# Kernel optimization log

Hardware: AMD Instinct MI355X
Metric: run time of the kernel (lower is better)

## Reference

```python
import jax, jax.numpy as jnp
import numpy as np

D_MODEL = 768
N_HEADS = 12
HEAD_DIM = D_MODEL // N_HEADS


def setup_inputs() -> dict:
    key = jax.random.key(0)
    k_x, k_wqkv, k_bqkv, k_wo, k_bo = jax.random.split(key, 5)
    s = 1.0 / np.sqrt(D_MODEL)
    return {
        "x": jax.random.normal(k_x, (4, 2048, D_MODEL), dtype=jnp.float32),
        "W_qkv": jax.random.uniform(k_wqkv, (D_MODEL, 3 * D_MODEL), jnp.float32, -s, s),
        "b_qkv": jax.random.uniform(k_bqkv, (3 * D_MODEL,), jnp.float32, -s, s),
        "W_out": jax.random.uniform(k_wo, (D_MODEL, D_MODEL), jnp.float32, -s, s),
        "b_out": jax.random.uniform(k_bo, (D_MODEL,), jnp.float32, -s, s),
    }


def reference(x, W_qkv, b_qkv, W_out, b_out):
    B, S, D = x.shape
    qkv = x @ W_qkv + b_qkv  # [B, S, 3D]
    q, k, v = jnp.split(qkv, 3, axis=-1)

    def heads(t):
        return t.reshape(B, S, N_HEADS, HEAD_DIM).transpose(0, 2, 1, 3)  # [B,H,S,Dh]

    q, k, v = heads(q), heads(k), heads(v)
    scale = HEAD_DIM ** -0.5
    scores = jnp.einsum("bhqd,bhkd->bhqk", q, k) * scale  # [B,H,S,S]
    causal = jnp.tril(jnp.ones((S, S), dtype=bool))
    scores = jnp.where(causal, scores, -jnp.inf)
    probs = jax.nn.softmax(scores, axis=-1)
    out = jnp.einsum("bhqk,bhkd->bhqd", probs, v)  # [B,H,S,Dh]
    out = out.transpose(0, 2, 1, 3).reshape(B, S, D)
    return out @ W_out + b_out
```

## Files before the change

kernel.cpp:

```cpp
#include <hip/hip_runtime.h>
#include <hip/hip_bf16.h>

#define D_MODEL 768
#define NH 12
#define HD 64
#define BATCH 4
#define SEQ 2048
#define BHN (BATCH*NH)
#define MROWS (BATCH*SEQ)

typedef unsigned short u16;
typedef unsigned int u32;
typedef __attribute__((ext_vector_type(8))) short short8;
typedef __attribute__((ext_vector_type(4))) float f32x4;

__device__ inline u16 f2bf(float f){
  union { __hip_bfloat16 h; u16 u; } cv; cv.h = __float2bfloat16(f); return cv.u;
}
__device__ inline u32 pack_bf2(float a, float b){
  return (u32)f2bf(a) | ((u32)f2bf(b) << 16);
}

__device__ inline void async_copy16(const void* g, void* l){
  __builtin_amdgcn_global_load_lds(
      (const __attribute__((address_space(1))) void*)g,
      (__attribute__((address_space(3))) void*)l, 16, 0, 0);
}

__global__ void cast4_kernel(const float* __restrict__ in, u16* __restrict__ out, int n4){
  int i = blockIdx.x*blockDim.x + threadIdx.x;
  if (i < n4){
    const float4 v = ((const float4*)in)[i];
    ushort4 o;
    o.x = f2bf(v.x); o.y = f2bf(v.y); o.z = f2bf(v.z); o.w = f2bf(v.w);
    ((ushort4*)out)[i] = o;
  }
}

__global__ void transpose_cast_kernel(const float* __restrict__ w, u16* __restrict__ wt,
                                      int K, int N){
  __shared__ u16 tile[64][65];
  int k0 = blockIdx.x*64, n0 = blockIdx.y*64;
  int c = threadIdx.x & 63, r0 = threadIdx.x >> 6;
  #pragma unroll
  for (int r = r0; r < 64; r += 4)
    tile[c][r] = f2bf(w[(size_t)(k0+r)*N + n0 + c]);
  __syncthreads();
  #pragma unroll
  for (int r = r0; r < 64; r += 4)
    wt[(size_t)(n0+r)*K + k0 + c] = tile[r][c];
}

template<int EPI>
__launch_bounds__(256)
__global__ void gemm_bf16(const u16* __restrict__ A, const u16* __restrict__ Bt,
                          const float* __restrict__ bias, float* __restrict__ outf,
                          u16* __restrict__ oq, u16* __restrict__ ok, u16* __restrict__ ovt,
                          int M, int N, int K)
{
  __shared__ alignas(16) char smem[32768];
  const int tid = threadIdx.x, wave = tid>>6, lane = tid&63;
  const int lr = lane&15, lg = lane>>4;
  const int m0 = blockIdx.x*128, n0 = blockIdx.y*128;
  const int wr = (wave>>1)*64, wc = (wave&1)*64;
  f32x4 acc[4][4] = {};
  const int srow = wave*32 + (lane>>2);
  const int schk = lane&3;

  auto stage = [&](int kt, int buf){
    char* Ab = smem + buf*8192;
    char* Bb = smem + 16384 + buf*8192;
    #pragma unroll
    for (int i = 0; i < 2; i++){
      int r = srow + i*16;
      async_copy16(A  + (size_t)(m0 + r)*K + kt + schk*8, Ab + (wave*32 + i*16)*64);
      async_copy16(Bt + (size_t)(n0 + r)*K + kt + schk*8, Bb + (wave*32 + i*16)*64);
    }
  };

  const int NT = K >> 5;
  stage(0, 0);
  for (int t = 0; t < NT; t++){
    const int c = t & 1;
    asm volatile("s_waitcnt vmcnt(0)" ::: "memory");
    __builtin_amdgcn_s_barrier();
    if (t+1 < NT) stage((t+1)<<5, c^1);

    const char* Ac = smem + c*8192;
    const char* Bc = smem + 16384 + c*8192;
    short8 a[4], b[4];
    #pragma unroll
    for (int mi = 0; mi < 4; mi++)
      a[mi] = *(const short8*)(Ac + (wr + mi*16 + lr)*64 + lg*16);
    #pragma unroll
    for (int ni = 0; ni < 4; ni++)
      b[ni] = *(const short8*)(Bc + (wc + ni*16 + lr)*64 + lg*16);
    #pragma unroll
    for (int mi = 0; mi < 4; mi++)
      #pragma unroll
      for (int ni = 0; ni < 4; ni++)
        acc[mi][ni] = __builtin_amdgcn_mfma_f32_16x16x32_bf16(a[mi], b[ni], acc[mi][ni], 0, 0, 0);
    asm volatile("s_waitcnt lgkmcnt(0)" ::: "memory");
    __builtin_amdgcn_sched_barrier(0);
    __builtin_amdgcn_s_barrier();
  }

  #pragma unroll
  for (int mi = 0; mi < 4; mi++)
  #pragma unroll
  for (int ni = 0; ni < 4; ni++)
  #pragma unroll
  for (int j = 0; j < 4; j++){
    int m = m0 + wr + mi*16 + lg*4 + j;
    int n = n0 + wc + ni*16 + lr;
    float v = acc[mi][ni][j] + bias[n];
    if (EPI == 0){
      outf[(size_t)m*N + n] = v;
    } else {
      int b_ = m >> 11, s = m & 2047;
      int t  = (n >= 1536) ? 2 : (n >= 768 ? 1 : 0);
      int hn = n - t*768;
      int h = hn >> 6, d = hn & 63;
      size_t base = (size_t)(b_*NH + h);
      if (t == 0)      oq [(base*SEQ + s)*HD + d] = f2bf(v * 0.1803368801f);
      else if (t == 1) ok [(base*SEQ + s)*HD + d] = f2bf(v);
      else             ovt[(base*HD + d)*SEQ + s] = f2bf(v);
    }
  }
}

__launch_bounds__(128, 2)
__global__ void attn_kernel(const u16* __restrict__ q, const u16* __restrict__ k,
                            const u16* __restrict__ vt, u16* __restrict__ aout)
{
  __shared__ alignas(16) char smem[43008];

  const int b1 = blockIdx.x;
  const int xcd = b1 & 7, grp = b1 >> 3;
  const int bh = xcd*6 + (grp >> 4);
  const int pairblk = grp & 15;
  const int tid = threadIdx.x, wave = tid>>6, lane = tid&63;
  const int lr = lane&15, lg = lane>>4;
  const int b_ = bh / NH, h_ = bh % NH;
  const u16* qp = q  + (size_t)bh*SEQ*HD;
  const u16* kp = k  + (size_t)bh*SEQ*HD;
  const u16* vp = vt + (size_t)bh*HD*SEQ;
  char* Pw = smem + 32768 + wave*5120;
  const int fswz = (lr&7)<<4;
  const int c8s = (lane&7) ^ (lane>>3);

  auto stageKV = [&](int kv0, int buf){
    char* Kb = smem + buf*16384;
    char* Vb = Kb + 8192;
    #pragma unroll
    for (int r = 0; r < 4; r++){
      int row = r*16 + wave*8 + (lane>>3);
      async_copy16(kp + (size_t)(kv0 + row)*HD + c8s*8, Kb + r*2048 + wave*1024);
      async_copy16(vp + (size_t)row*SEQ + kv0 + c8s*8,  Vb + r*2048 + wave*1024);
    }
  };

  #pragma unroll 1
  for (int half = 0; half < 2; half++){
    const int t = half ? (31 - pairblk) : pairblk;
    const int nkv = t + 1;
    const int q0w = t*64 + wave*32;

    short8 bq[2][2];
    #pragma unroll
    for (int h = 0; h < 2; h++)
      #pragma unroll
      for (int ks = 0; ks < 2; ks++)
        bq[h][ks] = *(const short8*)(qp + (size_t)(q0w + h*16 + lr)*HD + ks*32 + lg*8);

    float mrow[2] = {-INFINITY, -INFINITY};
    float lsum[2] = {0.f, 0.f};
    f32x4 o[4][2] = {};

    asm volatile("s_waitcnt vmcnt(0) lgkmcnt(0)" ::: "memory");
    __builtin_amdgcn_sched_barrier(0);
    __builtin_amdgcn_s_barrier();
    stageKV(0, 0);

    #pragma unroll 1
    for (int kvb = 0; kvb < nkv; kvb++){
      const int c = kvb & 1;
      const int kv0 = kvb*64;
      asm volatile("s_waitcnt vmcnt(0) lgkmcnt(0)" ::: "memory");
      __builtin_amdgcn_sched_barrier(0);
      __builtin_amdgcn_s_barrier();
      if (kvb+1 < nkv) stageKV(kv0 + 64, c^1);

      const char* Kb = smem + c*16384;
      const char* Vb = Kb + 8192;

      f32x4 s[4][2] = {};
      __builtin_amdgcn_s_setprio(1);
      #pragma unroll
      for (int ni = 0; ni < 4; ni++){
        short8 k0 = *(const short8*)(Kb + (ni*16+lr)*128 + ((lg*16) ^ fswz));
        short8 k1 = *(const short8*)(Kb + (ni*16+lr)*128 + ((64 + lg*16) ^ fswz));
        #pragma unroll
        for (int h = 0; h < 2; h++){
          s[ni][h] = __builtin_amdgcn_mfma_f32_16x16x32_bf16(k0, bq[h][0], s[ni][h], 0,0,0);
          s[ni][h] = __builtin_amdgcn_mfma_f32_16x16x32_bf16(k1, bq[h][1], s[ni][h], 0,0,0);
        }
      }
      __builtin_amdgcn_s_setprio(0);

      if (kvb == nkv-1){
        #pragma unroll
        for (int ni = 0; ni < 4; ni++)
          #pragma unroll
          for (int h = 0; h < 2; h++)
            #pragma unroll
            for (int jj = 0; jj < 4; jj++){
              int col = kv0 + ni*16 + lg*4 + jj;
              int qrow = q0w + h*16 + lr;
              if (col > qrow) s[ni][h][jj] = -1e30f;
            }
      }

      #pragma unroll
      for (int h = 0; h < 2; h++){
        float v0 = fmaxf(fmaxf(s[0][h][0], s[0][h][1]), fmaxf(s[0][h][2], s[0][h][3]));
        float v1 = fmaxf(fmaxf(s[1][h][0], s[1][h][1]), fmaxf(s[1][h][2], s[1][h][3]));
        float v2 = fmaxf(fmaxf(s[2][h][0], s[2][h][1]), fmaxf(s[2][h][2], s[2][h][3]));
        float v3 = fmaxf(fmaxf(s[3][h][0], s[3][h][1]), fmaxf(s[3][h][2], s[3][h][3]));
        float vloc = fmaxf(fmaxf(v0, v1), fmaxf(v2, v3));
        if (!__all(vloc - mrow[h] <= 8.0f)){
          float v = fmaxf(vloc, __shfl_xor(vloc, 16));
          v = fmaxf(v, __shfl_xor(v, 32));
          float mn = fmaxf(mrow[h], v);
          float alpha = __builtin_amdgcn_exp2f(mrow[h] - mn);
          mrow[h] = mn;
          lsum[h] *= alpha;
          #pragma unroll
          for (int ni = 0; ni < 4; ni++)
            #pragma unroll
            for (int jj = 0; jj < 4; jj++)
              o[ni][h][jj] *= alpha;
        }
        const float mn = mrow[h];
        char* hb = Pw + h*2560;
        float psum = 0.f;
        #pragma unroll
        for (int ni = 0; ni < 4; ni++){
          float p0 = __builtin_amdgcn_exp2f(s[ni][h][0] - mn);
          float p1 = __builtin_amdgcn_exp2f(s[ni][h][1] - mn);
          float p2 = __builtin_amdgcn_exp2f(s[ni][h][2] - mn);
          float p3 = __builtin_amdgcn_exp2f(s[ni][h][3] - mn);
          psum += (p0+p1) + (p2+p3);
          int tl = lr + 16*(((ni&1)<<1) | (lg>>1));
          int wb = ((ni>>1)<<2) | ((lg&1)<<1);
          *(u32*)(hb + tl*40 + wb*4)     = pack_bf2(p0, p1);
          *(u32*)(hb + tl*40 + wb*4 + 4) = pack_bf2(p2, p3);
        }
        lsum[h] += psum;
      }

      union { u32 w[4]; short8 v; } pb[2][2];
      #pragma unroll
      for (int h = 0; h < 2; h++)
        #pragma unroll
        for (int ks = 0; ks < 2; ks++){
          const char* hb = Pw + h*2560 + (size_t)lane*40 + ks*16;
          pb[h][ks].w[0] = *(const u32*)(hb);
          pb[h][ks].w[1] = *(const u32*)(hb + 4);
          pb[h][ks].w[2] = *(const u32*)(hb + 8);
          pb[h][ks].w[3] = *(const u32*)(hb + 12);
        }

      __builtin_amdgcn_s_setprio(1);
      #pragma unroll
      for (int ni = 0; ni < 4; ni++){
        short8 v0 = *(const short8*)(Vb + (ni*16+lr)*128 + ((lg*16) ^ fswz));
        short8 v1 = *(const short8*)(Vb + (ni*16+lr)*128 + ((64 + lg*16) ^ fswz));
        #pragma unroll
        for (int h = 0; h < 2; h++){
          o[ni][h] = __builtin_amdgcn_mfma_f32_16x16x32_bf16(v0, pb[h][0].v, o[ni][h], 0,0,0);
          o[ni][h] = __builtin_amdgcn_mfma_f32_16x16x32_bf16(v1, pb[h][1].v, o[ni][h], 0,0,0);
        }
      }
      __builtin_amdgcn_s_setprio(0);
    }

    #pragma unroll
    for (int h = 0; h < 2; h++){
      float ls = lsum[h];
      ls += __shfl_xor(ls, 16);
      ls += __shfl_xor(ls, 32);
      float inv = 1.0f / ls;
      u16* orow = aout + ((size_t)b_*SEQ + q0w + h*16 + lr)*D_MODEL + h_*HD;
      #pragma unroll
      for (int ni = 0; ni < 4; ni++){
        ushort4 w;
        w.x = f2bf(o[ni][h][0]*inv);
        w.y = f2bf(o[ni][h][1]*inv);
        w.z = f2bf(o[ni][h][2]*inv);
        w.w = f2bf(o[ni][h][3]*inv);
        *(ushort4*)(orow + ni*16 + lg*4) = w;
      }
    }
  }
}

extern "C" void kernel_launch(void* const* d_in, const int* in_sizes, int n_in,
                              void* d_out, int out_size, void* d_ws, size_t ws_size,
                              hipStream_t stream)
{
  const float* x    = (const float*)d_in[0];
  const float* Wqkv = (const float*)d_in[1];
  const float* bqkv = (const float*)d_in[2];
  const float* Wout = (const float*)d_in[3];
  const float* bout = (const float*)d_in[4];
  float* out = (float*)d_out;
  char* ws = (char*)d_ws;

  u16* x_bf   = (u16*)(ws + 0);
  u16* wqkv_t = (u16*)(ws + 12582912);
  u16* wout_t = (u16*)(ws + 16121856);
  u16* qb     = (u16*)(ws + 17301504);
  u16* kb     = (u16*)(ws + 29884416);
  u16* vtb    = (u16*)(ws + 42467328);
  u16* attnb  = (u16*)(ws + 55050240);

  cast4_kernel<<<6144, 256, 0, stream>>>(x, x_bf, (BATCH*SEQ*D_MODEL)/4);
  transpose_cast_kernel<<<dim3(12, 36), 256, 0, stream>>>(Wqkv, wqkv_t, 768, 2304);
  transpose_cast_kernel<<<dim3(12, 12), 256, 0, stream>>>(Wout, wout_t, 768, 768);

  gemm_bf16<1><<<dim3(64, 18), 256, 0, stream>>>(x_bf, wqkv_t, bqkv, nullptr,
                                                 qb, kb, vtb, MROWS, 3*D_MODEL, D_MODEL);

  attn_kernel<<<768, 128, 0, stream>>>(qb, kb, vtb, attnb);

  gemm_bf16<0><<<dim3(64, 6), 256, 0, stream>>>(attnb, wout_t, bout, out,
                                                nullptr, nullptr, nullptr, MROWS, D_MODEL, D_MODEL);
}
```

Baseline: 150.7 us.

## Process paired causal query tiles jointly in one KV sweep with four waves

The attention kernel now uses 4 waves per block. Each wave owns 16 rows of the high query tile and 16 rows of the paired low tile. Previously two sequential halves each re-streamed K/V; now one KV loop serves both tiles until the low tile's diagonal, then continues for the high tile alone. This halves K/V staging for the shared prefix and raises waves per block, at the cost of more LDS per block and heavier register and occupancy pressure. The GEMM main loop also drops its trailing lgkmcnt wait and barrier, relying on the top-of-loop barrier to protect the double buffer.

```diff
diff --git a/kernel.cpp b/kernel.cpp
--- a/kernel.cpp
+++ b/kernel.cpp
@@ -100,9 +100,6 @@
       #pragma unroll
       for (int ni = 0; ni < 4; ni++)
         acc[mi][ni] = __builtin_amdgcn_mfma_f32_16x16x32_bf16(a[mi], b[ni], acc[mi][ni], 0, 0, 0);
-    asm volatile("s_waitcnt lgkmcnt(0)" ::: "memory");
-    __builtin_amdgcn_sched_barrier(0);
-    __builtin_amdgcn_s_barrier();
   }
 
   #pragma unroll
@@ -129,16 +126,17 @@
   }
 }
 
-__launch_bounds__(128, 2)
+__launch_bounds__(256, 3)
 __global__ void attn_kernel(const u16* __restrict__ q, const u16* __restrict__ k,
                             const u16* __restrict__ vt, u16* __restrict__ aout)
 {
-  __shared__ alignas(16) char smem[43008];
+  __shared__ alignas(16) char smem[53248];
 
   const int b1 = blockIdx.x;
   const int xcd = b1 & 7, grp = b1 >> 3;
   const int bh = xcd*6 + (grp >> 4);
-  const int pairblk = grp & 15;
+  const int p  = grp & 15;
+  const int hi = 31 - p;
   const int tid = threadIdx.x, wave = tid>>6, lane = tid&63;
   const int lr = lane&15, lg = lane>>4;
   const int b_ = bh / NH, h_ = bh % NH;
@@ -148,159 +146,193 @@
   char* Pw = smem + 32768 + wave*5120;
   const int fswz = (lr&7)<<4;
   const int c8s = (lane&7) ^ (lane>>3);
+  const int nkv = hi + 1;
 
   auto stageKV = [&](int kv0, int buf){
     char* Kb = smem + buf*16384;
     char* Vb = Kb + 8192;
     #pragma unroll
-    for (int r = 0; r < 4; r++){
-      int row = r*16 + wave*8 + (lane>>3);
-      async_copy16(kp + (size_t)(kv0 + row)*HD + c8s*8, Kb + r*2048 + wave*1024);
-      async_copy16(vp + (size_t)row*SEQ + kv0 + c8s*8,  Vb + r*2048 + wave*1024);
+    for (int r = 0; r < 2; r++){
+      int row = wave*16 + r*8 + (lane>>3);
+      async_copy16(kp + (size_t)(kv0 + row)*HD + c8s*8, Kb + (wave*16 + r*8)*128);
+      async_copy16(vp + (size_t)row*SEQ + kv0 + c8s*8,  Vb + (wave*16 + r*8)*128);
     }
   };
 
+  const int qrow[2] = { hi*64 + wave*16 + lr, p*64 + wave*16 + lr };
+
+  short8 bq[2][2];
+  #pragma unroll
+  for (int h = 0; h < 2; h++)
+    #pragma unroll
+    for (int ks = 0; ks < 2; ks++)
+      bq[h][ks] = *(const short8*)(qp + (size_t)qrow[h]*HD + ks*32 + lg*8);
+
+  float mrow[2] = {-INFINITY, -INFINITY};
+  float lsum[2] = {0.f, 0.f};
+  f32x4 o[4][2] = {};
+
+  stageKV(0, 0);
+
+  auto softmax_pack = [&](f32x4 (&s)[4][2], int h, bool domask, int kv0, int qr){
+    if (domask){
+      #pragma unroll
+      for (int ni = 0; ni < 4; ni++)
+        #pragma unroll
+        for (int jj = 0; jj < 4; jj++){
+          int col = kv0 + ni*16 + lg*4 + jj;
+          if (col > qr) s[ni][h][jj] = -1e30f;
+        }
+    }
+    float v0 = fmaxf(fmaxf(s[0][h][0], s[0][h][1]), fmaxf(s[0][h][2], s[0][h][3]));
+    float v1 = fmaxf(fmaxf(s[1][h][0], s[1][h][1]), fmaxf(s[1][h][2], s[1][h][3]));
+    float v2 = fmaxf(fmaxf(s[2][h][0], s[2][h][1]), fmaxf(s[2][h][2], s[2][h][3]));
+    float v3 = fmaxf(fmaxf(s[3][h][0], s[3][h][1]), fmaxf(s[3][h][2], s[3][h][3]));
+    float vloc = fmaxf(fmaxf(v0, v1), fmaxf(v2, v3));
+    if (!__all(vloc - mrow[h] <= 8.0f)){
+      float v = fmaxf(vloc, __shfl_xor(vloc, 16));
+      v = fmaxf(v, __shfl_xor(v, 32));
+      float mn = fmaxf(mrow[h], v);
+      float alpha = __builtin_amdgcn_exp2f(mrow[h] - mn);
+      mrow[h] = mn;
+      lsum[h] *= alpha;
+      #pragma unroll
+      for (int ni = 0; ni < 4; ni++)
+        #pragma unroll
+        for (int jj = 0; jj < 4; jj++)
+          o[ni][h][jj] *= alpha;
+    }
+    const float mn = mrow[h];
+    char* hb = Pw + h*2560;
+    float psum = 0.f;
+    #pragma unroll
+    for (int ni = 0; ni < 4; ni++){
+      float p0 = __builtin_amdgcn_exp2f(s[ni][h][0] - mn);
+      float p1 = __builtin_amdgcn_exp2f(s[ni][h][1] - mn);
+      float p2 = __builtin_amdgcn_exp2f(s[ni][h][2] - mn);
+      float p3 = __builtin_amdgcn_exp2f(s[ni][h][3] - mn);
+      psum += (p0+p1) + (p2+p3);
+      int tl = lr + 16*(((ni&1)<<1) | (lg>>1));
+      int wb = ((ni>>1)<<2) | ((lg&1)<<1);
+      *(u32*)(hb + tl*40 + wb*4)     = pack_bf2(p0, p1);
+      *(u32*)(hb + tl*40 + wb*4 + 4) = pack_bf2(p2, p3);
+    }
+    lsum[h] += psum;
+  };
+
+  auto read_pb = [&](int h, short8& r0, short8& r1){
+    const char* hb = Pw + h*2560 + (size_t)lane*40;
+    union { u32 w[4]; short8 v; } a, b;
+    a.w[0] = *(const u32*)(hb);      a.w[1] = *(const u32*)(hb + 4);
+    a.w[2] = *(const u32*)(hb + 8);  a.w[3] = *(const u32*)(hb + 12);
+    b.w[0] = *(const u32*)(hb + 16); b.w[1] = *(const u32*)(hb + 20);
+    b.w[2] = *(const u32*)(hb + 24); b.w[3] = *(const u32*)(hb + 28);
+    r0 = a.v; r1 = b.v;
+  };
+
+  int kvb = 0;
+
   #pragma unroll 1
-  for (int half = 0; half < 2; half++){
-    const int t = half ? (31 - pairblk) : pairblk;
-    const int nkv = t + 1;
-    const int q0w = t*64 + wave*32;
-
-    short8 bq[2][2];
-    #pragma unroll
-    for (int h = 0; h < 2; h++)
-      #pragma unroll
-      for (int ks = 0; ks < 2; ks++)
-        bq[h][ks] = *(const short8*)(qp + (size_t)(q0w + h*16 + lr)*HD + ks*32 + lg*8);
-
-    float mrow[2] = {-INFINITY, -INFINITY};
-    float lsum[2] = {0.f, 0.f};
-    f32x4 o[4][2] = {};
-
-    asm volatile("s_waitcnt vmcnt(0) lgkmcnt(0)" ::: "memory");
-    __builtin_amdgcn_sched_barrier(0);
+  for (; kvb <= p; kvb++){
+    const int c = kvb & 1;
+    const int kv0 = kvb*64;
+    asm volatile("s_waitcnt vmcnt(0)" ::: "memory");
     __builtin_amdgcn_s_barrier();
-    stageKV(0, 0);
-
-    #pragma unroll 1
-    for (int kvb = 0; kvb < nkv; kvb++){
-      const int c = kvb & 1;
-      const int kv0 = kvb*64;
-      asm volatile("s_waitcnt vmcnt(0) lgkmcnt(0)" ::: "memory");
-      __builtin_amdgcn_sched_barrier(0);
-      __builtin_amdgcn_s_barrier();
-      if (kvb+1 < nkv) stageKV(kv0 + 64, c^1);
-
-      const char* Kb = smem + c*16384;
-      const char* Vb = Kb + 8192;
-
-      f32x4 s[4][2] = {};
-      __builtin_amdgcn_s_setprio(1);
-      #pragma unroll
-      for (int ni = 0; ni < 4; ni++){
-        short8 k0 = *(const short8*)(Kb + (ni*16+lr)*128 + ((lg*16) ^ fswz));
-        short8 k1 = *(const short8*)(Kb + (ni*16+lr)*128 + ((64 + lg*16) ^ fswz));
-        #pragma unroll
-        for (int h = 0; h < 2; h++){
-          s[ni][h] = __builtin_amdgcn_mfma_f32_16x16x32_bf16(k0, bq[h][0], s[ni][h], 0,0,0);
-          s[ni][h] = __builtin_amdgcn_mfma_f32_16x16x32_bf16(k1, bq[h][1], s[ni][h], 0,0,0);
-        }
+    if (kvb+1 < nkv) stageKV(kv0 + 64, c^1);
+
+    const char* Kb = smem + c*16384;
+    const char* Vb = Kb + 8192;
+
+    f32x4 s[4][2] = {};
+    __builtin_amdgcn_s_setprio(1);
+    #pragma unroll
+    for (int ni = 0; ni < 4; ni++){
+      short8 k0 = *(const short8*)(Kb + (ni*16+lr)*128 + ((lg*16) ^ fswz));
+      short8 k1 = *(const short8*)(Kb + (ni*16+lr)*128 + ((64 + lg*16) ^ fswz));
+      #pragma unroll
+      for (int h = 0; h < 2; h++){
+        s[ni][h] = __builtin_amdgcn_mfma_f32_16x16x32_bf16(k0, bq[h][0], s[ni][h], 0,0,0);
+        s[ni][h] = __builtin_amdgcn_mfma_f32_16x16x32_bf16(k1, bq[h][1], s[ni][h], 0,0,0);
       }
-      __builtin_amdgcn_s_setprio(0);
-
-      if (kvb == nkv-1){
-        #pragma unroll
-        for (int ni = 0; ni < 4; ni++)
-          #pragma unroll
-          for (int h = 0; h < 2; h++)
-            #pragma unroll
-            for (int jj = 0; jj < 4; jj++){
-              int col = kv0 + ni*16 + lg*4 + jj;
-              int qrow = q0w + h*16 + lr;
-              if (col > qrow) s[ni][h][jj] = -1e30f;
-            }
+    }
+    __builtin_amdgcn_s_setprio(0);
+
+    softmax_pack(s, 0, false, kv0, qrow[0]);
+    softmax_pack(s, 1, kvb == p, kv0, qrow[1]);
+
+    short8 pb[2][2];
+    read_pb(0, pb[0][0], pb[0][1]);
+    read_pb(1, pb[1][0], pb[1][1]);
+
+    __builtin_amdgcn_s_setprio(1);
+    #pragma unroll
+    for (int ni = 0; ni < 4; ni++){
+      short8 v0 = *(const short8*)(Vb + (ni*16+lr)*128 + ((lg*16) ^ fswz));
+      short8 v1 = *(const short8*)(Vb + (ni*16+lr)*128 + ((64 + lg*16) ^ fswz));
+      #pragma unroll
+      for (int h = 0; h < 2; h++){
+        o[ni][h] = __builtin_amdgcn_mfma_f32_16x16x32_bf16(v0, pb[h][0], o[ni][h], 0,0,0);
+        o[ni][h] = __builtin_amdgcn_mfma_f32_16x16x32_bf16(v1, pb[h][1], o[ni][h], 0,0,0);
       }
-
-      #pragma unroll
-      for (int h = 0; h < 2; h++){
-        float v0 = fmaxf(fmaxf(s[0][h][0], s[0][h][1]), fmaxf(s[0][h][2], s[0][h][3]));
-        float v1 = fmaxf(fmaxf(s[1][h][0], s[1][h][1]), fmaxf(s[1][h][2], s[1][h][3]));
-        float v2 = fmaxf(fmaxf(s[2][h][0], s[2][h][1]), fmaxf(s[2][h][2], s[2][h][3]));
-        float v3 = fmaxf(fmaxf(s[3][h][0], s[3][h][1]), fmaxf(s[3][h][2], s[3][h][3]));
-        float vloc = fmaxf(fmaxf(v0, v1), fmaxf(v2, v3));
-        if (!__all(vloc - mrow[h] <= 8.0f)){
-          float v = fmaxf(vloc, __shfl_xor(vloc, 16));
-          v = fmaxf(v, __shfl_xor(v, 32));
-          float mn = fmaxf(mrow[h], v);
-          float alpha = __builtin_amdgcn_exp2f(mrow[h] - mn);
-          mrow[h] = mn;
-          lsum[h] *= alpha;
-          #pragma unroll
-          for (int ni = 0; ni < 4; ni++)
-            #pragma unroll
-            for (int jj = 0; jj < 4; jj++)
-              o[ni][h][jj] *= alpha;
-        }
-        const float mn = mrow[h];
-        char* hb = Pw + h*2560;
-        float psum = 0.f;
-        #pragma unroll
-        for (int ni = 0; ni < 4; ni++){
-          float p0 = __builtin_amdgcn_exp2f(s[ni][h][0] - mn);
-          float p1 = __builtin_amdgcn_exp2f(s[ni][h][1] - mn);
-          float p2 = __builtin_amdgcn_exp2f(s[ni][h][2] - mn);
-          float p3 = __builtin_amdgcn_exp2f(s[ni][h][3] - mn);
-          psum += (p0+p1) + (p2+p3);
-          int tl = lr + 16*(((ni&1)<<1) | (lg>>1));
-          int wb = ((ni>>1)<<2) | ((lg&1)<<1);
-          *(u32*)(hb + tl*40 + wb*4)     = pack_bf2(p0, p1);
-          *(u32*)(hb + tl*40 + wb*4 + 4) = pack_bf2(p2, p3);
-        }
-        lsum[h] += psum;
-      }
-
-      union { u32 w[4]; short8 v; } pb[2][2];
-      #pragma unroll
-      for (int h = 0; h < 2; h++)
-        #pragma unroll
-        for (int ks = 0; ks < 2; ks++){
-          const char* hb = Pw + h*2560 + (size_t)lane*40 + ks*16;
-          pb[h][ks].w[0] = *(const u32*)(hb);
-          pb[h][ks].w[1] = *(const u32*)(hb + 4);
-          pb[h][ks].w[2] = *(const u32*)(hb + 8);
-          pb[h][ks].w[3] = *(const u32*)(hb + 12);
-        }
-
-      __builtin_amdgcn_s_setprio(1);
-      #pragma unroll
-      for (int ni = 0; ni < 4; ni++){
-        short8 v0 = *(const short8*)(Vb + (ni*16+lr)*128 + ((lg*16) ^ fswz));
-        short8 v1 = *(const short8*)(Vb + (ni*16+lr)*128 + ((64 + lg*16) ^ fswz));
-        #pragma unroll
-        for (int h = 0; h < 2; h++){
-          o[ni][h] = __builtin_amdgcn_mfma_f32_16x16x32_bf16(v0, pb[h][0].v, o[ni][h], 0,0,0);
-          o[ni][h] = __builtin_amdgcn_mfma_f32_16x16x32_bf16(v1, pb[h][1].v, o[ni][h], 0,0,0);
-        }
-      }
-      __builtin_amdgcn_s_setprio(0);
-    }
-
-    #pragma unroll
-    for (int h = 0; h < 2; h++){
-      float ls = lsum[h];
-      ls += __shfl_xor(ls, 16);
-      ls += __shfl_xor(ls, 32);
-      float inv = 1.0f / ls;
-      u16* orow = aout + ((size_t)b_*SEQ + q0w + h*16 + lr)*D_MODEL + h_*HD;
-      #pragma unroll
-      for (int ni = 0; ni < 4; ni++){
-        ushort4 w;
-        w.x = f2bf(o[ni][h][0]*inv);
-        w.y = f2bf(o[ni][h][1]*inv);
-        w.z = f2bf(o[ni][h][2]*inv);
-        w.w = f2bf(o[ni][h][3]*inv);
-        *(ushort4*)(orow + ni*16 + lg*4) = w;
-      }
+    }
+    __builtin_amdgcn_s_setprio(0);
+  }
+
+  #pragma unroll 1
+  for (; kvb < nkv; kvb++){
+    const int c = kvb & 1;
+    const int kv0 = kvb*64;
+    asm volatile("s_waitcnt vmcnt(0)" ::: "memory");
+    __builtin_amdgcn_s_barrier();
+    if (kvb+1 < nkv) stageKV(kv0 + 64, c^1);
+
+    const char* Kb = smem + c*16384;
+    const char* Vb = Kb + 8192;
+
+    f32x4 s[4][2];
+    #pragma unroll
+    for (int ni = 0; ni < 4; ni++) s[ni][0] = (f32x4){0.f,0.f,0.f,0.f};
+    __builtin_amdgcn_s_setprio(1);
+    #pragma unroll
+    for (int ni = 0; ni < 4; ni++){
+      short8 k0 = *(const short8*)(Kb + (ni*16+lr)*128 + ((lg*16) ^ fswz));
+      short8 k1 = *(const short8*)(Kb + (ni*16+lr)*128 + ((64 + lg*16) ^ fswz));
+      s[ni][0] = __builtin_amdgcn_mfma_f32_16x16x32_bf16(k0, bq[0][0], s[ni][0], 0,0,0);
+      s[ni][0] = __builtin_amdgcn_mfma_f32_16x16x32_bf16(k1, bq[0][1], s[ni][0], 0,0,0);
+    }
+    __builtin_amdgcn_s_setprio(0);
+
+    softmax_pack(s, 0, kvb == hi, kv0, qrow[0]);
+
+    short8 pb0, pb1;
+    read_pb(0, pb0, pb1);
+
+    __builtin_amdgcn_s_setprio(1);
+    #pragma unroll
+    for (int ni = 0; ni < 4; ni++){
+      short8 v0 = *(const short8*)(Vb + (ni*16+lr)*128 + ((lg*16) ^ fswz));
+      short8 v1 = *(const short8*)(Vb + (ni*16+lr)*128 + ((64 + lg*16) ^ fswz));
+      o[ni][0] = __builtin_amdgcn_mfma_f32_16x16x32_bf16(v0, pb0, o[ni][0], 0,0,0);
+      o[ni][0] = __builtin_amdgcn_mfma_f32_16x16x32_bf16(v1, pb1, o[ni][0], 0,0,0);
+    }
+    __builtin_amdgcn_s_setprio(0);
+  }
+
+  #pragma unroll
+  for (int h = 0; h < 2; h++){
+    float ls = lsum[h];
+    ls += __shfl_xor(ls, 16);
+    ls += __shfl_xor(ls, 32);
+    float inv = 1.0f / ls;
+    u16* orow = aout + ((size_t)b_*SEQ + qrow[h])*D_MODEL + h_*HD;
+    #pragma unroll
+    for (int ni = 0; ni < 4; ni++){
+      ushort4 w;
+      w.x = f2bf(o[ni][h][0]*inv);
+      w.y = f2bf(o[ni][h][1]*inv);
+      w.z = f2bf(o[ni][h][2]*inv);
+      w.w = f2bf(o[ni][h][3]*inv);
+      *(ushort4*)(orow + ni*16 + lg*4) = w;
     }
   }
 }
@@ -332,7 +364,7 @@
   gemm_bf16<1><<<dim3(64, 18), 256, 0, stream>>>(x_bf, wqkv_t, bqkv, nullptr,
                                                  qb, kb, vtb, MROWS, 3*D_MODEL, D_MODEL);
 
-  attn_kernel<<<768, 128, 0, stream>>>(qb, kb, vtb, attnb);
+  attn_kernel<<<768, 256, 0, stream>>>(qb, kb, vtb, attnb);
 
   gemm_bf16<0><<<dim3(64, 6), 256, 0, stream>>>(attnb, wout_t, bout, out,
                                                 nullptr, nullptr, nullptr, MROWS, D_MODEL, D_MODEL);
```

Result: faster. 138.8 us (-7.9%).
